# Optimization experiments

Hardware: AMD Instinct MI355X
Metric: run time of the kernel (lower is better)

The kernel has to match this reference:

```python
import jax, jax.numpy as jnp
import numpy as np

N_QUBITS = 10
DEPTH = 4
BATCH = 2048


def _ry(state, theta, q, n):
    # RY(theta) = [[cos(t/2), -sin(t/2)], [sin(t/2), cos(t/2)]], per-sample theta [B]
    B = state.shape[0]
    st = state.reshape(B, 2 ** q, 2, 2 ** (n - q - 1))
    c = jnp.cos(theta * 0.5)[:, None, None]
    s = jnp.sin(theta * 0.5)[:, None, None]
    a0, a1 = st[:, :, 0], st[:, :, 1]
    out = jnp.stack([c * a0 - s * a1, s * a0 + c * a1], axis=2)
    return out.reshape(B, -1)


def _rx(state, theta, q, n):
    # RX(theta) = [[cos(t/2), -i sin(t/2)], [-i sin(t/2), cos(t/2)]], shared scalar theta
    B = state.shape[0]
    st = state.reshape(B, 2 ** q, 2, 2 ** (n - q - 1))
    c = jnp.cos(theta * 0.5)
    s = jnp.sin(theta * 0.5)
    a0, a1 = st[:, :, 0], st[:, :, 1]
    out = jnp.stack([c * a0 - 1j * s * a1, -1j * s * a0 + c * a1], axis=2)
    return out.reshape(B, -1)


def _cnot(state, ctrl, tgt, n):
    # flip target amplitudes in the control=1 subspace
    B = state.shape[0]
    lo, hi = min(ctrl, tgt), max(ctrl, tgt)
    st = state.reshape(B, 2 ** lo, 2, 2 ** (hi - lo - 1), 2, 2 ** (n - hi - 1))
    if ctrl == lo:
        s0 = st[:, :, 0]                      # [B, 2^lo, mid, 2, rest]
        s1 = jnp.flip(st[:, :, 1], axis=3)    # flip target (axis 3 after indexing)
        out = jnp.stack([s0, s1], axis=2)
    else:
        s0 = st[:, :, :, :, 0]                # [B, 2^lo, 2, mid, rest]
        s1 = jnp.flip(st[:, :, :, :, 1], axis=2)  # flip target (axis 2)
        out = jnp.stack([s0, s1], axis=4)
    return out.reshape(B, -1)


def _circuit(x, w):
    B, n = x.shape
    depth = w.shape[0]
    state = jnp.zeros((B, 2 ** n), dtype=jnp.complex64).at[:, 0].set(1.0)
    # AngleEmbedding with RY rotations, per-sample angles
    for q in range(n):
        state = _ry(state, x[:, q], q, n)
    # BasicEntanglerLayers: RX on every wire, then CNOT ring
    for l in range(depth):
        for q in range(n):
            state = _rx(state, w[l, q], q, n)
        if n == 2:
            state = _cnot(state, 0, 1, n)
        else:
            for q in range(n):
                state = _cnot(state, q, (q + 1) % n, n)
    probs = state.real ** 2 + state.imag ** 2  # [B, 2^n]
    zs = []
    for q in range(n):
        m = probs.reshape(B, 2 ** q, 2, -1).sum(axis=(1, 3))  # marginal over wire q
        zs.append(m[:, 0] - m[:, 1])
    return jnp.stack(zs, axis=1)  # [B, n]


def setup_inputs() -> dict:
    key = jax.random.key(0)
    kx, kw = jax.random.split(key)
    x = jax.random.normal(kx, (BATCH, N_QUBITS), dtype=jnp.float32)
    q_weights = 0.02 * jax.random.normal(kw, (DEPTH, N_QUBITS), dtype=jnp.float32)
    return {"x": x, "q_weights": q_weights}


def reference(x, q_weights):
    return _circuit(x, q_weights)
```

## Files before the change

kernel.cpp:

```cpp
#include <hip/hip_runtime.h>

#define NQ 10
#define NDEPTH 4
#define NR 16


__device__ __forceinline__ float xf(int i) { return __int_as_float(i); }
__device__ __forceinline__ int   fx(float f) { return __float_as_int(f); }

template<int M>
__device__ __forceinline__ float lane_xor(float v, int a32) {
    if constexpr (M == 1)
        return xf(__builtin_amdgcn_update_dpp(fx(v), fx(v), 0xB1, 0xF, 0xF, true));
    else if constexpr (M == 2)
        return xf(__builtin_amdgcn_update_dpp(fx(v), fx(v), 0x4E, 0xF, 0xF, true));
    else if constexpr (M == 8)
        return xf(__builtin_amdgcn_update_dpp(fx(v), fx(v), 0x128, 0xF, 0xF, true));
    else if constexpr (M == 4)
        return xf(__builtin_amdgcn_ds_swizzle(fx(v), 0x101F));
    else if constexpr (M == 16)
        return xf(__builtin_amdgcn_ds_swizzle(fx(v), 0x401F));
    else
        return xf(__builtin_amdgcn_ds_bpermute(a32, fx(v)));
}

__global__ __launch_bounds__(256, 2) void vql_kernel(
    const float* __restrict__ x,
    const float* __restrict__ w,
    float* __restrict__ out,
    int B)
{
    const int lane = threadIdx.x & 63;
    const int b = blockIdx.x * 4 + (threadIdx.x >> 6);
    if (b >= B) return;
    const int a32 = (lane ^ 32) << 2;

    const float2* xr = reinterpret_cast<const float2*>(x + b * NQ);
    const float2 x01 = xr[0], x23 = xr[1], x45 = xr[2], x67 = xr[3], x89 = xr[4];
    const float xa[NQ] = {0.5f * x01.x, 0.5f * x01.y, 0.5f * x23.x, 0.5f * x23.y,
                          0.5f * x45.x, 0.5f * x45.y, 0.5f * x67.x, 0.5f * x67.y,
                          0.5f * x89.x, 0.5f * x89.y};

    float F0r[NQ], F0i[NQ], F1r[NQ], F1i[NQ];
    #pragma unroll
    for (int q = 0; q < NQ; ++q) {
        float sy, cy, s, c;
        __sincosf(xa[q], &sy, &cy);
        __sincosf(0.5f * w[q], &s, &c);
        const float v0r = c * cy,  v0i = -s * sy;
        const float v1r = c * sy,  v1i = -s * cy;
        F0r[q] = v0r + v1r;  F0i[q] = v0i + v1i;
        F1r[q] = v0r - v1r;  F1i[q] = v0i - v1i;
    }

    const int L0 = lane & 1,        L1 = (lane >> 1) & 1, L2 = (lane >> 2) & 1;
    const int L3 = (lane >> 3) & 1, L4 = (lane >> 4) & 1, L5 = (lane >> 5) & 1;
    const int PL1 = L0 ^ L1, PL2 = PL1 ^ L2, PL3 = PL2 ^ L3, PL4 = PL3 ^ L4;
    const int g[7] = {PL4, PL4 ^ L5, PL3 ^ L5, PL2 ^ L5, PL1 ^ L5, L0 ^ L5, L5};
    #define SR_(q,bit) ((bit) ? F1r[q] : F0r[q])
    #define SI_(q,bit) ((bit) ? F1i[q] : F0i[q])

    float A_r[2], A_i[2];
    #pragma unroll
    for (int t = 0; t < 2; ++t) {
        float ar = SR_(0, g[0] ^ t), ai = SI_(0, g[0] ^ t);
        #pragma unroll
        for (int q = 1; q < 7; ++q) {
            const float br = SR_(q, g[q] ^ t), bi = SI_(q, g[q] ^ t);
            const float nr = ar * br - ai * bi;
            const float ni = ar * bi + ai * br;
            ar = nr; ai = ni;
        }
        A_r[t] = ar * (1.0f / 1024.0f);
        A_i[t] = ai * (1.0f / 1024.0f);
    }
    float Gr[2][2], Gi[2][2];
    #pragma unroll
    for (int t2 = 0; t2 < 2; ++t2)
        #pragma unroll
        for (int t1 = 0; t1 < 2; ++t1) {
            const float ar = SR_(8, t2 ^ L5), ai = SI_(8, t2 ^ L5);
            const float br = SR_(9, t1 ^ L5), bi = SI_(9, t1 ^ L5);
            Gr[t2][t1] = ar * br - ai * bi;
            Gi[t2][t1] = ar * bi + ai * br;
        }
    float Br_[2][2][2], Bi_[2][2][2];
    #pragma unroll
    for (int t3 = 0; t3 < 2; ++t3)
        #pragma unroll
        for (int t2 = 0; t2 < 2; ++t2)
            #pragma unroll
            for (int t1 = 0; t1 < 2; ++t1) {
                const float ar = SR_(7, t3 ^ L5), ai = SI_(7, t3 ^ L5);
                Br_[t3][t2][t1] = ar * Gr[t2][t1] - ai * Gi[t2][t1];
                Bi_[t3][t2][t1] = ar * Gi[t2][t1] + ai * Gr[t2][t1];
            }
    float re[NR], im[NR];
    #pragma unroll
    for (int r = 0; r < NR; ++r) {
        const int r0 = r & 1, r1 = (r >> 1) & 1, r2 = (r >> 2) & 1, r3 = (r >> 3) & 1;
        const int p1 = r0, p2 = r0 ^ r1, p3 = p2 ^ r2, p4 = p3 ^ r3;
        const float br = Br_[p3][p2][p1], bi = Bi_[p3][p2][p1];
        re[r] = A_r[p4] * br - A_i[p4] * bi;
        im[r] = A_r[p4] * bi + A_i[p4] * br;
    }
    #undef SR_
    #undef SI_

    float h1[NQ], h2[NQ], h3[NQ];
    #pragma unroll
    for (int q = 0; q < NQ; ++q) {
        h1[q] = 0.5f * w[NQ + q];
        h2[q] = 0.5f * w[2 * NQ + q];
        h3[q] = 0.5f * w[3 * NQ + q];
    }
    #define SG_(M) ((__builtin_popcount(lane & (M)) & 1) ? -1.f : 1.f)
    const float s1 = SG_(1),  s2 = SG_(2),  s3 = SG_(3),  s4 = SG_(4),  s5 = SG_(5);
    const float s6 = SG_(6),  s8 = SG_(8),  s10 = SG_(10), s12 = SG_(12);
    const float s16 = SG_(16), s20 = SG_(20), s24 = SG_(24), s32 = SG_(32);
    const float s40 = SG_(40), s48 = SG_(48);
    #undef SG_

    float C[NR];
    C[0]  = s32 * h1[0] + s16 * h1[1] + s8 * h1[2] + s4 * h1[3] + s2 * h1[4] + s1 * h1[5]
          + s48 * h2[0] + s24 * h2[1] + s12 * h2[2] + s6 * h2[3] + s3 * h2[4]
          + s40 * h3[0] + s20 * h3[1] + s10 * h3[2] + s5 * h3[3];
    C[8]  = h1[6] + s1 * h2[5] + s2 * h3[4];
    C[4]  = h1[7] + s1 * h3[5];
    C[2]  = h1[8] + s48 * h3[8];
    C[1]  = h1[9] + s48 * h2[9] + s24 * h3[9];
    C[12] = h2[6];
    C[6]  = h2[7];
    C[3]  = h2[8];
    C[10] = h3[6];
    C[5]  = h3[7];
    C[7] = 0.f; C[9] = 0.f; C[11] = 0.f; C[13] = 0.f; C[14] = 0.f; C[15] = 0.f;

    #pragma unroll
    for (int bset = 0; bset < 4; ++bset) {
        const int bb = 1 << bset;
        #pragma unroll
        for (int r = 0; r < NR; ++r) {
            if (!(r & bb)) {
                const float u = C[r], v = C[r | bb];
                C[r] = u + v;  C[r | bb] = u - v;
            }
        }
    }
    #pragma unroll
    for (int r = 0; r < NR; ++r) {
        float sp, cp;
        __sincosf(C[r], &sp, &cp);
        const float nr = re[r] * cp + im[r] * sp;
        const float ni = im[r] * cp - re[r] * sp;
        re[r] = nr; im[r] = ni;
    }

    #pragma unroll
    for (int bset = 0; bset < 4; ++bset) {
        const int bb = 1 << bset;
        #pragma unroll
        for (int r = 0; r < NR; ++r) {
            if (!(r & bb)) {
                float u = re[r], v = re[r | bb];
                re[r] = u + v;  re[r | bb] = u - v;
                u = im[r]; v = im[r | bb];
                im[r] = u + v;  im[r | bb] = u - v;
            }
        }
    }
    {
        const float sgA = (lane &  1) ? -1.f : 1.f;
        const float sgB = (lane &  2) ? -1.f : 1.f;
        const float sgC = (lane &  4) ? -1.f : 1.f;
        const float sgD = (lane &  8) ? -1.f : 1.f;
        const float sgE = (lane & 16) ? -1.f : 1.f;
        const float sgF = (lane & 32) ? -1.f : 1.f;
        #pragma unroll
        for (int r = 0; r < NR; ++r) {
            float p;
            p = lane_xor< 1>(re[r], a32); re[r] = fmaf(sgA, re[r], p);
            p = lane_xor< 1>(im[r], a32); im[r] = fmaf(sgA, im[r], p);
            p = lane_xor< 2>(re[r], a32); re[r] = fmaf(sgB, re[r], p);
            p = lane_xor< 2>(im[r], a32); im[r] = fmaf(sgB, im[r], p);
            p = lane_xor< 4>(re[r], a32); re[r] = fmaf(sgC, re[r], p);
            p = lane_xor< 4>(im[r], a32); im[r] = fmaf(sgC, im[r], p);
            p = lane_xor< 8>(re[r], a32); re[r] = fmaf(sgD, re[r], p);
            p = lane_xor< 8>(im[r], a32); im[r] = fmaf(sgD, im[r], p);
            p = lane_xor<16>(re[r], a32); re[r] = fmaf(sgE, re[r], p);
            p = lane_xor<16>(im[r], a32); im[r] = fmaf(sgE, im[r], p);
            p = lane_xor<32>(re[r], a32); re[r] = fmaf(sgF, re[r], p);
            p = lane_xor<32>(im[r], a32); im[r] = fmaf(sgF, im[r], p);
        }
    }

    float W[NR];
    #pragma unroll
    for (int r = 0; r < NR; ++r) W[r] = re[r] * re[r] + im[r] * im[r];
    #pragma unroll
    for (int bset = 0; bset < 4; ++bset) {
        const int bb = 1 << bset;
        #pragma unroll
        for (int r = 0; r < NR; ++r) {
            if (!(r & bb)) {
                const float u = W[r], v = W[r | bb];
                W[r] = u + v;  W[r | bb] = u - v;
            }
        }
    }
    const float sg44 = (__builtin_popcount(lane & 44) & 1) ? -1.f : 1.f;
    const float sg26 = (__builtin_popcount(lane & 26) & 1) ? -1.f : 1.f;
    const float sg13 = (__builtin_popcount(lane & 13) & 1) ? -1.f : 1.f;
    const float sg38 = (__builtin_popcount(lane & 38) & 1) ? -1.f : 1.f;
    const float sg51 = (__builtin_popcount(lane & 51) & 1) ? -1.f : 1.f;
    const float sg25 = (__builtin_popcount(lane & 25) & 1) ? -1.f : 1.f;
    const float sg12 = (__builtin_popcount(lane & 12) & 1) ? -1.f : 1.f;

    float z[NQ];
    z[0] = sg44 * W[12];
    z[1] = sg26 * W[10];
    z[2] = sg13 * W[ 5];
    z[3] = sg38 * W[10];
    z[4] = sg51 * W[ 5];
    z[5] = sg25 * W[10];
    z[6] = sg12 * W[13];
    z[7] = sg38 * W[ 6];
    z[8] = sg51 * W[ 3];
    z[9] = sg25 * W[ 9];

    #pragma unroll
    for (int q = 0; q < NQ; ++q) {
        z[q] += lane_xor< 1>(z[q], a32);
        z[q] += lane_xor< 2>(z[q], a32);
        z[q] += lane_xor< 4>(z[q], a32);
        z[q] += lane_xor< 8>(z[q], a32);
        z[q] += lane_xor<16>(z[q], a32);
        z[q] += lane_xor<32>(z[q], a32);
    }
    if (lane == 0) {
        #pragma unroll
        for (int q = 0; q < NQ; ++q) out[b * NQ + q] = z[q];
    }
}

extern "C" void kernel_launch(void* const* d_in, const int* in_sizes, int n_in,
                              void* d_out, int out_size, void* d_ws, size_t ws_size,
                              hipStream_t stream) {
    const float* x = (const float*)d_in[0];
    const float* w = (const float*)d_in[1];
    float* out = (float*)d_out;
    const int B = in_sizes[0] / NQ;
    vql_kernel<<<(B + 3) / 4, 256, 0, stream>>>(x, w, out, B);
}
```

Before: 11.44 us.

## Split each sample's statevector across two wavefronts with LDS butterfly exchange

```diff
diff --git a/kernel.cpp b/kernel.cpp
--- a/kernel.cpp
+++ b/kernel.cpp
@@ -1,8 +1,7 @@
 #include <hip/hip_runtime.h>
 
 #define NQ 10
-#define NDEPTH 4
-#define NR 16
+#define NR 8
 
 
 __device__ __forceinline__ float xf(int i) { return __int_as_float(i); }
@@ -24,16 +23,20 @@
         return xf(__builtin_amdgcn_ds_bpermute(a32, fx(v)));
 }
 
-__global__ __launch_bounds__(256, 2) void vql_kernel(
+__global__ __launch_bounds__(256, 4) void vql_kernel(
     const float* __restrict__ x,
     const float* __restrict__ w,
-    float* __restrict__ out,
-    int B)
+    float* __restrict__ out)
 {
-    const int lane = threadIdx.x & 63;
-    const int b = blockIdx.x * 4 + (threadIdx.x >> 6);
-    if (b >= B) return;
-    const int a32 = (lane ^ 32) << 2;
+    __shared__ float4 xch[2][2][4][64];
+    __shared__ float  zbuf[2][2][NQ];
+
+    const int tid  = threadIdx.x;
+    const int lane = tid & 63;
+    const int wv   = (tid >> 6) & 1;
+    const int eb   = tid >> 7;
+    const int b    = blockIdx.x * 2 + eb;
+    const int a32  = (lane ^ 32) << 2;
 
     const float2* xr = reinterpret_cast<const float2*>(x + b * NQ);
     const float2 x01 = xr[0], x23 = xr[1], x45 = xr[2], x67 = xr[3], x89 = xr[4];
@@ -55,18 +58,18 @@
 
     const int L0 = lane & 1,        L1 = (lane >> 1) & 1, L2 = (lane >> 2) & 1;
     const int L3 = (lane >> 3) & 1, L4 = (lane >> 4) & 1, L5 = (lane >> 5) & 1;
-    const int PL1 = L0 ^ L1, PL2 = PL1 ^ L2, PL3 = PL2 ^ L3, PL4 = PL3 ^ L4;
-    const int g[7] = {PL4, PL4 ^ L5, PL3 ^ L5, PL2 ^ L5, PL1 ^ L5, L0 ^ L5, L5};
+    const int PL1 = L0 ^ L1, PL2 = PL1 ^ L2, PL3 = PL2 ^ L3, PL4 = PL3 ^ L4, PL5 = PL4 ^ L5;
+    const int gb[8] = {PL5, PL5 ^ wv, PL4 ^ wv, PL3 ^ wv, PL2 ^ wv, PL1 ^ wv, L0 ^ wv, wv};
     #define SR_(q,bit) ((bit) ? F1r[q] : F0r[q])
     #define SI_(q,bit) ((bit) ? F1i[q] : F0i[q])
 
     float A_r[2], A_i[2];
     #pragma unroll
     for (int t = 0; t < 2; ++t) {
-        float ar = SR_(0, g[0] ^ t), ai = SI_(0, g[0] ^ t);
-        #pragma unroll
-        for (int q = 1; q < 7; ++q) {
-            const float br = SR_(q, g[q] ^ t), bi = SI_(q, g[q] ^ t);
+        float ar = SR_(0, gb[0] ^ t), ai = SI_(0, gb[0] ^ t);
+        #pragma unroll
+        for (int q = 1; q < 8; ++q) {
+            const float br = SR_(q, gb[q] ^ t), bi = SI_(q, gb[q] ^ t);
             const float nr = ar * br - ai * bi;
             const float ni = ar * bi + ai * br;
             ar = nr; ai = ni;
@@ -79,30 +82,19 @@
     for (int t2 = 0; t2 < 2; ++t2)
         #pragma unroll
         for (int t1 = 0; t1 < 2; ++t1) {
-            const float ar = SR_(8, t2 ^ L5), ai = SI_(8, t2 ^ L5);
-            const float br = SR_(9, t1 ^ L5), bi = SI_(9, t1 ^ L5);
+            const float ar = SR_(8, t2 ^ wv), ai = SI_(8, t2 ^ wv);
+            const float br = SR_(9, t1 ^ wv), bi = SI_(9, t1 ^ wv);
             Gr[t2][t1] = ar * br - ai * bi;
             Gi[t2][t1] = ar * bi + ai * br;
         }
-    float Br_[2][2][2], Bi_[2][2][2];
-    #pragma unroll
-    for (int t3 = 0; t3 < 2; ++t3)
-        #pragma unroll
-        for (int t2 = 0; t2 < 2; ++t2)
-            #pragma unroll
-            for (int t1 = 0; t1 < 2; ++t1) {
-                const float ar = SR_(7, t3 ^ L5), ai = SI_(7, t3 ^ L5);
-                Br_[t3][t2][t1] = ar * Gr[t2][t1] - ai * Gi[t2][t1];
-                Bi_[t3][t2][t1] = ar * Gi[t2][t1] + ai * Gr[t2][t1];
-            }
     float re[NR], im[NR];
     #pragma unroll
     for (int r = 0; r < NR; ++r) {
-        const int r0 = r & 1, r1 = (r >> 1) & 1, r2 = (r >> 2) & 1, r3 = (r >> 3) & 1;
-        const int p1 = r0, p2 = r0 ^ r1, p3 = p2 ^ r2, p4 = p3 ^ r3;
-        const float br = Br_[p3][p2][p1], bi = Bi_[p3][p2][p1];
-        re[r] = A_r[p4] * br - A_i[p4] * bi;
-        im[r] = A_r[p4] * bi + A_i[p4] * br;
+        const int r0 = r & 1, r1 = (r >> 1) & 1, r2 = (r >> 2) & 1;
+        const int rp2 = r0 ^ r1, rq3 = rp2 ^ r2;
+        const float gr = Gr[rp2][r0], gi = Gi[rp2][r0];
+        re[r] = A_r[rq3] * gr - A_i[rq3] * gi;
+        im[r] = A_r[rq3] * gi + A_i[rq3] * gr;
     }
     #undef SR_
     #undef SI_
@@ -115,29 +107,28 @@
         h3[q] = 0.5f * w[3 * NQ + q];
     }
     #define SG_(M) ((__builtin_popcount(lane & (M)) & 1) ? -1.f : 1.f)
-    const float s1 = SG_(1),  s2 = SG_(2),  s3 = SG_(3),  s4 = SG_(4),  s5 = SG_(5);
-    const float s6 = SG_(6),  s8 = SG_(8),  s10 = SG_(10), s12 = SG_(12);
-    const float s16 = SG_(16), s20 = SG_(20), s24 = SG_(24), s32 = SG_(32);
-    const float s40 = SG_(40), s48 = SG_(48);
-    #undef SG_
+    const float g1 = SG_(1),  g2 = SG_(2),  g3 = SG_(3),  g4 = SG_(4),  g5 = SG_(5);
+    const float g6 = SG_(6),  g8 = SG_(8),  g10 = SG_(10), g12 = SG_(12);
+    const float g16 = SG_(16), g20 = SG_(20), g24 = SG_(24), g32 = SG_(32);
+    const float g40 = SG_(40), g48 = SG_(48);
+    const float sw = wv ? -1.f : 1.f;
 
     float C[NR];
-    C[0]  = s32 * h1[0] + s16 * h1[1] + s8 * h1[2] + s4 * h1[3] + s2 * h1[4] + s1 * h1[5]
-          + s48 * h2[0] + s24 * h2[1] + s12 * h2[2] + s6 * h2[3] + s3 * h2[4]
-          + s40 * h3[0] + s20 * h3[1] + s10 * h3[2] + s5 * h3[3];
-    C[8]  = h1[6] + s1 * h2[5] + s2 * h3[4];
-    C[4]  = h1[7] + s1 * h3[5];
-    C[2]  = h1[8] + s48 * h3[8];
-    C[1]  = h1[9] + s48 * h2[9] + s24 * h3[9];
-    C[12] = h2[6];
-    C[6]  = h2[7];
-    C[3]  = h2[8];
-    C[10] = h3[6];
-    C[5]  = h3[7];
-    C[7] = 0.f; C[9] = 0.f; C[11] = 0.f; C[13] = 0.f; C[14] = 0.f; C[15] = 0.f;
-
-    #pragma unroll
-    for (int bset = 0; bset < 4; ++bset) {
+    C[0] = sw * h1[0] + g32 * h1[1] + g16 * h1[2] + g8 * h1[3] + g4 * h1[4]
+         + g2 * h1[5] + g1 * h1[6]
+         + sw * g32 * h2[0] + g48 * h2[1] + g24 * h2[2] + g12 * h2[3]
+         + g6 * h2[4] + g3 * h2[5]
+         + sw * g16 * h3[0] + g40 * h3[1] + g20 * h3[2] + g10 * h3[3] + g5 * h3[4];
+    C[4] = h1[7] + g1 * h2[6] + g2 * h3[5];
+    C[2] = h1[8] + g1 * h3[6] + sw * g32 * h3[8];
+    C[1] = h1[9] + sw * g32 * h2[9] + g48 * h3[9];
+    C[6] = h2[7];
+    C[3] = h2[8];
+    C[5] = h3[7];
+    C[7] = 0.f;
+
+    #pragma unroll
+    for (int bset = 0; bset < 3; ++bset) {
         const int bb = 1 << bset;
         #pragma unroll
         for (int r = 0; r < NR; ++r) {
@@ -157,7 +148,7 @@
     }
 
     #pragma unroll
-    for (int bset = 0; bset < 4; ++bset) {
+    for (int bset = 0; bset < 3; ++bset) {
         const int bb = 1 << bset;
         #pragma unroll
         for (int r = 0; r < NR; ++r) {
@@ -193,40 +184,53 @@
             p = lane_xor<32>(im[r], a32); im[r] = fmaf(sgF, im[r], p);
         }
     }
-
-    float W[NR];
-    #pragma unroll
-    for (int r = 0; r < NR; ++r) W[r] = re[r] * re[r] + im[r] * im[r];
-    #pragma unroll
-    for (int bset = 0; bset < 4; ++bset) {
+    xch[eb][wv][0][lane] = make_float4(re[0], re[1], re[2], re[3]);
+    xch[eb][wv][1][lane] = make_float4(re[4], re[5], re[6], re[7]);
+    xch[eb][wv][2][lane] = make_float4(im[0], im[1], im[2], im[3]);
+    xch[eb][wv][3][lane] = make_float4(im[4], im[5], im[6], im[7]);
+    __syncthreads();
+    {
+        const float4 pr0 = xch[eb][wv ^ 1][0][lane], pr1 = xch[eb][wv ^ 1][1][lane];
+        const float4 pi0 = xch[eb][wv ^ 1][2][lane], pi1 = xch[eb][wv ^ 1][3][lane];
+        const float prre[NR] = {pr0.x, pr0.y, pr0.z, pr0.w, pr1.x, pr1.y, pr1.z, pr1.w};
+        const float prim[NR] = {pi0.x, pi0.y, pi0.z, pi0.w, pi1.x, pi1.y, pi1.z, pi1.w};
+        const float sgW = wv ? -1.f : 1.f;
+        #pragma unroll
+        for (int r = 0; r < NR; ++r) {
+            re[r] = fmaf(sgW, re[r], prre[r]);
+            im[r] = fmaf(sgW, im[r], prim[r]);
+        }
+    }
+
+    float P[NR];
+    #pragma unroll
+    for (int r = 0; r < NR; ++r) P[r] = re[r] * re[r] + im[r] * im[r];
+    #pragma unroll
+    for (int bset = 0; bset < 3; ++bset) {
         const int bb = 1 << bset;
         #pragma unroll
         for (int r = 0; r < NR; ++r) {
             if (!(r & bb)) {
-                const float u = W[r], v = W[r | bb];
-                W[r] = u + v;  W[r | bb] = u - v;
+                const float u = P[r], v = P[r | bb];
+                P[r] = u + v;  P[r | bb] = u - v;
             }
         }
     }
-    const float sg44 = (__builtin_popcount(lane & 44) & 1) ? -1.f : 1.f;
-    const float sg26 = (__builtin_popcount(lane & 26) & 1) ? -1.f : 1.f;
-    const float sg13 = (__builtin_popcount(lane & 13) & 1) ? -1.f : 1.f;
-    const float sg38 = (__builtin_popcount(lane & 38) & 1) ? -1.f : 1.f;
-    const float sg51 = (__builtin_popcount(lane & 51) & 1) ? -1.f : 1.f;
-    const float sg25 = (__builtin_popcount(lane & 25) & 1) ? -1.f : 1.f;
-    const float sg12 = (__builtin_popcount(lane & 12) & 1) ? -1.f : 1.f;
+    const float q25 = SG_(25), q53 = SG_(53), q26 = SG_(26), q13 = SG_(13);
+    const float q38 = SG_(38), q51 = SG_(51), q12 = SG_(12);
+    #undef SG_
 
     float z[NQ];
-    z[0] = sg44 * W[12];
-    z[1] = sg26 * W[10];
-    z[2] = sg13 * W[ 5];
-    z[3] = sg38 * W[10];
-    z[4] = sg51 * W[ 5];
-    z[5] = sg25 * W[10];
-    z[6] = sg12 * W[13];
-    z[7] = sg38 * W[ 6];
-    z[8] = sg51 * W[ 3];
-    z[9] = sg25 * W[ 9];
+    z[0] = sw * q25 * P[4];
+    z[1] = q53 * P[2];
+    z[2] = q26 * P[5];
+    z[3] = sw * q13 * P[2];
+    z[4] = sw * q38 * P[5];
+    z[5] = q51 * P[2];
+    z[6] = q25 * P[5];
+    z[7] = sw * q12 * P[6];
+    z[8] = sw * q38 * P[3];
+    z[9] = q51 * P[1];
 
     #pragma unroll
     for (int q = 0; q < NQ; ++q) {
@@ -239,7 +243,12 @@
     }
     if (lane == 0) {
         #pragma unroll
-        for (int q = 0; q < NQ; ++q) out[b * NQ + q] = z[q];
+        for (int q = 0; q < NQ; ++q) zbuf[eb][wv][q] = z[q];
+    }
+    __syncthreads();
+    if (wv == 0 && lane == 0) {
+        #pragma unroll
+        for (int q = 0; q < NQ; ++q) out[b * NQ + q] = z[q] + zbuf[eb][1][q];
     }
 }
 
@@ -250,5 +259,5 @@
     const float* w = (const float*)d_in[1];
     float* out = (float*)d_out;
     const int B = in_sizes[0] / NQ;
-    vql_kernel<<<(B + 3) / 4, 256, 0, stream>>>(x, w, out, B);
+    vql_kernel<<<B / 2, 256, 0, stream>>>(x, w, out);
 }
```

Result: slower. 12.92 us (+12.9%).

## Precompute weight-only phase table in a separate kernel and load it per lane

Applied to the files above, without the earlier changes.

```diff
diff --git a/kernel.cpp b/kernel.cpp
--- a/kernel.cpp
+++ b/kernel.cpp
@@ -1,7 +1,6 @@
 #include <hip/hip_runtime.h>
 
 #define NQ 10
-#define NDEPTH 4
 #define NR 16
 
 
@@ -24,9 +23,32 @@
         return xf(__builtin_amdgcn_ds_bpermute(a32, fx(v)));
 }
 
+__global__ __launch_bounds__(256) void phase_kernel(
+    const float* __restrict__ w, float2* __restrict__ tbl)
+{
+    const int k = blockIdx.x * 256 + threadIdx.x;
+    const int M[30] = {512,256,128,64,32,16,8,4,2,1,
+                       768,384,192,96,48,24,12,6,3,769,
+                       640,320,160,80,40,20,10,5,770,385};
+    float phi = 0.f;
+    #pragma unroll
+    for (int i = 0; i < 30; ++i) {
+        const float h = 0.5f * w[10 + i];
+        phi += (__builtin_popcount(k & M[i]) & 1) ? -h : h;
+    }
+    float sp, cp;
+    __sincosf(phi, &sp, &cp);
+    tbl[k] = make_float2(cp, sp);
+    if (k < NQ) {
+        float s, c;
+        __sincosf(0.5f * w[k], &s, &c);
+        tbl[1024 + k] = make_float2(c, s);
+    }
+}
+
 __global__ __launch_bounds__(256, 2) void vql_kernel(
     const float* __restrict__ x,
-    const float* __restrict__ w,
+    const float2* __restrict__ tbl,
     float* __restrict__ out,
     int B)
 {
@@ -35,6 +57,13 @@
     if (b >= B) return;
     const int a32 = (lane ^ 32) << 2;
 
+    float2 E[NR];
+    {
+        const float2* tb = tbl + (lane << 4);
+        #pragma unroll
+        for (int r = 0; r < NR; ++r) E[r] = tb[r];
+    }
+
     const float2* xr = reinterpret_cast<const float2*>(x + b * NQ);
     const float2 x01 = xr[0], x23 = xr[1], x45 = xr[2], x67 = xr[3], x89 = xr[4];
     const float xa[NQ] = {0.5f * x01.x, 0.5f * x01.y, 0.5f * x23.x, 0.5f * x23.y,
@@ -44,11 +73,11 @@
     float F0r[NQ], F0i[NQ], F1r[NQ], F1i[NQ];
     #pragma unroll
     for (int q = 0; q < NQ; ++q) {
-        float sy, cy, s, c;
+        float sy, cy;
         __sincosf(xa[q], &sy, &cy);
-        __sincosf(0.5f * w[q], &s, &c);
-        const float v0r = c * cy,  v0i = -s * sy;
-        const float v1r = c * sy,  v1i = -s * cy;
+        const float2 w0 = tbl[1024 + q];
+        const float v0r = w0.x * cy,  v0i = -w0.y * sy;
+        const float v1r = w0.x * sy,  v1i = -w0.y * cy;
         F0r[q] = v0r + v1r;  F0i[q] = v0i + v1i;
         F1r[q] = v0r - v1r;  F1i[q] = v0i - v1i;
     }
@@ -107,50 +136,9 @@
     #undef SR_
     #undef SI_
 
-    float h1[NQ], h2[NQ], h3[NQ];
-    #pragma unroll
-    for (int q = 0; q < NQ; ++q) {
-        h1[q] = 0.5f * w[NQ + q];
-        h2[q] = 0.5f * w[2 * NQ + q];
-        h3[q] = 0.5f * w[3 * NQ + q];
-    }
-    #define SG_(M) ((__builtin_popcount(lane & (M)) & 1) ? -1.f : 1.f)
-    const float s1 = SG_(1),  s2 = SG_(2),  s3 = SG_(3),  s4 = SG_(4),  s5 = SG_(5);
-    const float s6 = SG_(6),  s8 = SG_(8),  s10 = SG_(10), s12 = SG_(12);
-    const float s16 = SG_(16), s20 = SG_(20), s24 = SG_(24), s32 = SG_(32);
-    const float s40 = SG_(40), s48 = SG_(48);
-    #undef SG_
-
-    float C[NR];
-    C[0]  = s32 * h1[0] + s16 * h1[1] + s8 * h1[2] + s4 * h1[3] + s2 * h1[4] + s1 * h1[5]
-          + s48 * h2[0] + s24 * h2[1] + s12 * h2[2] + s6 * h2[3] + s3 * h2[4]
-          + s40 * h3[0] + s20 * h3[1] + s10 * h3[2] + s5 * h3[3];
-    C[8]  = h1[6] + s1 * h2[5] + s2 * h3[4];
-    C[4]  = h1[7] + s1 * h3[5];
-    C[2]  = h1[8] + s48 * h3[8];
-    C[1]  = h1[9] + s48 * h2[9] + s24 * h3[9];
-    C[12] = h2[6];
-    C[6]  = h2[7];
-    C[3]  = h2[8];
-    C[10] = h3[6];
-    C[5]  = h3[7];
-    C[7] = 0.f; C[9] = 0.f; C[11] = 0.f; C[13] = 0.f; C[14] = 0.f; C[15] = 0.f;
-
-    #pragma unroll
-    for (int bset = 0; bset < 4; ++bset) {
-        const int bb = 1 << bset;
-        #pragma unroll
-        for (int r = 0; r < NR; ++r) {
-            if (!(r & bb)) {
-                const float u = C[r], v = C[r | bb];
-                C[r] = u + v;  C[r | bb] = u - v;
-            }
-        }
-    }
     #pragma unroll
     for (int r = 0; r < NR; ++r) {
-        float sp, cp;
-        __sincosf(C[r], &sp, &cp);
+        const float cp = E[r].x, sp = E[r].y;
         const float nr = re[r] * cp + im[r] * sp;
         const float ni = im[r] * cp - re[r] * sp;
         re[r] = nr; im[r] = ni;
@@ -230,10 +218,10 @@
 
     #pragma unroll
     for (int q = 0; q < NQ; ++q) {
-        z[q] += lane_xor< 1>(z[q], a32);
-        z[q] += lane_xor< 2>(z[q], a32);
-        z[q] += lane_xor< 4>(z[q], a32);
-        z[q] += lane_xor< 8>(z[q], a32);
+        z[q] += lane_xor<1>(z[q], a32);
+        z[q] += lane_xor<2>(z[q], a32);
+        z[q] += lane_xor<4>(z[q], a32);
+        z[q] += lane_xor<8>(z[q], a32);
         z[q] += lane_xor<16>(z[q], a32);
         z[q] += lane_xor<32>(z[q], a32);
     }
@@ -249,6 +237,8 @@
     const float* x = (const float*)d_in[0];
     const float* w = (const float*)d_in[1];
     float* out = (float*)d_out;
+    float2* tbl = (float2*)d_ws;
     const int B = in_sizes[0] / NQ;
-    vql_kernel<<<(B + 3) / 4, 256, 0, stream>>>(x, w, out, B);
-}
+    phase_kernel<<<4, 256, 0, stream>>>(w, tbl);
+    vql_kernel<<<(B + 3) / 4, 256, 0, stream>>>(x, tbl, out, B);
+}
```

New measurement: 16.58 us. 44.9% more time.
